# Optimization experiments

Hardware: AMD Instinct MI355X
Metric: run time of the kernel (lower is better)

Reference implementation:

```python
import jax, jax.numpy as jnp
import numpy as np

# Qwen3-MoE style config
B, S, D = 2, 2048, 2048        # batch, seqlen, hidden_size
E, I, TOPK = 64, 768, 8        # num_experts, moe_intermediate_size, num_experts_per_tok
M = B * S                      # tokens
CAP = 2 * (M * TOPK) // E


def setup_inputs() -> dict:
    key = jax.random.key(0)
    k0, k1, k2, k3, k4 = jax.random.split(key, 5)
    return {
        "x": jax.random.normal(k0, (B, S, D), jnp.float32),
        "router_weight": jax.random.normal(k1, (D, E), jnp.float32) * 0.02,
        "gate_proj": jax.random.normal(k2, (E, D, I), jnp.float32) * 0.02,
        "up_proj": jax.random.normal(k3, (E, D, I), jnp.float32) * 0.02,
        "down_proj": jax.random.normal(k4, (E, I, D), jnp.float32) * 0.02,
    }


def _moe(x, router_weight, gate_proj, up_proj, down_proj):
    b, s, d = x.shape
    xf = x.reshape(-1, d)                                  # [M, d]
    m = xf.shape[0]

    # ---- TokenChoiceTopKRouter: softmax scores, top-k, renormalize ----
    logits = xf @ router_weight                            # [M, E]
    probs = jax.nn.softmax(logits.astype(jnp.float32), axis=-1)
    topw, topi = jax.lax.top_k(probs, TOPK)                # [M, k]
    topw = topw / topw.sum(axis=-1, keepdims=True)         # norm_topk_prob

    flat_e = topi.reshape(-1)                              # [M*k] expert id per assignment
    flat_w = topw.reshape(-1).astype(x.dtype)              # [M*k] routing weight per assignment

    # ---- permute: sort assignments by expert (stable) ----
    order = jnp.argsort(flat_e)                            # [M*k]
    se = flat_e[order]                                     # sorted expert ids
    tok = order // TOPK                                    # source token per sorted assignment
    counts = jax.ops.segment_sum(jnp.ones_like(flat_e), flat_e, num_segments=E)
    starts = jnp.cumsum(counts) - counts                   # exclusive prefix sum
    pos = jnp.arange(m * TOPK) - starts[se]                # slot within expert's buffer
    valid = pos < CAP
    posc = jnp.minimum(pos, CAP - 1)

    # ---- dispatch to padded per-expert buffers [E, CAP, d] ----
    xe = jnp.zeros((E, CAP, d), x.dtype).at[se, pos].set(xf[tok], mode='drop')

    # ---- grouped SwiGLU experts (batched GEMMs) ----
    h = jax.nn.silu(jnp.einsum('ecd,edi->eci', xe, gate_proj)) \
        * jnp.einsum('ecd,edi->eci', xe, up_proj)          # [E, CAP, I]
    ye = jnp.einsum('eci,eid->ecd', h, down_proj)          # [E, CAP, d]

    # ---- unpermute + weighted combine ----
    contrib = jnp.where(valid[:, None], ye[se, posc], 0.0) * flat_w[order][:, None]
    out = jnp.zeros((m, d), x.dtype).at[tok].add(contrib)  # sum over topk per token
    return out.reshape(b, s, d)


def reference(x, router_weight, gate_proj, up_proj, down_proj):
    return _moe(x, router_weight, gate_proj, up_proj, down_proj)
```

## Files before the change

### kernel.cpp

```cpp
#include <hip/hip_runtime.h>
#include <hip/hip_bf16.h>

typedef __attribute__((ext_vector_type(4))) float f32x4;
typedef __attribute__((ext_vector_type(8))) short bf16x8;
typedef __attribute__((ext_vector_type(8))) unsigned short us8;
typedef unsigned int   u32;
typedef unsigned short u16;

#define D_DIM 2048
#define I_DIM 768
#define NE    64
#define CAP   1024
#define NTOK  4096

__device__ __forceinline__ u32 cvt2(float a, float b) {
  __hip_bfloat162 hh = __float22bfloat162_rn(float2{a, b});
  union { __hip_bfloat162 h; u32 u; } c; c.h = hh; return c.u;
}
__device__ __forceinline__ u16 f2b(float f) {
  __hip_bfloat16 b = __float2bfloat16(f);
  union { __hip_bfloat16 b; u16 u; } c; c.b = b; return c.u;
}
__device__ __forceinline__ float b2f(u16 v) {
  union { u32 u; float f; } c; c.u = (u32)v << 16; return c.f;
}
__device__ __forceinline__ void glp16(const void* g, void* l) {
  __builtin_amdgcn_global_load_lds(
      (const __attribute__((address_space(1))) u32*)g,
      (__attribute__((address_space(3))) u32*)l, 16, 0, 0);
}

#define VMW(n) asm volatile("s_waitcnt vmcnt(" #n ")" ::: "memory")
#define BARF   do { __builtin_amdgcn_s_barrier(); \
                    asm volatile("" ::: "memory"); } while (0)

__global__ __launch_bounds__(256) void k_cvt_x(const float* __restrict__ x,
                                               u16* __restrict__ xb) {
  const size_t i = ((size_t)blockIdx.x * 256 + threadIdx.x) * 8;
  float4 v0 = *(const float4*)(x + i);
  float4 v1 = *(const float4*)(x + i + 4);
  uint4 o;
  o.x = cvt2(v0.x, v0.y); o.y = cvt2(v0.z, v0.w);
  o.z = cvt2(v1.x, v1.y); o.w = cvt2(v1.z, v1.w);
  *(uint4*)(xb + i) = o;
}

__global__ __launch_bounds__(256) void k_router(
    const float* __restrict__ x, const float* __restrict__ rw,
    int* __restrict__ counts, int* __restrict__ slot_token,
    float* __restrict__ slot_w)
{
  const int lane = threadIdx.x & 63;
  const int tok  = blockIdx.x * 4 + (threadIdx.x >> 6);
  const float* xr = x + (size_t)tok * D_DIM;

  float acc = 0.f;
  for (int d0 = 0; d0 < D_DIM; d0 += 64) {
    float xv = xr[d0 + lane];
    #pragma unroll
    for (int j = 0; j < 64; ++j) {
      float xj = __shfl(xv, j, 64);
      acc = fmaf(xj, rw[(size_t)(d0 + j) * NE + lane], acc);
    }
  }

  float v = acc; int vi = lane;
  float wk[8]; int ei[8];
  float mx0 = 0.f, wsum = 0.f;
  #pragma unroll
  for (int k = 0; k < 8; ++k) {
    float mv = v; int mi = vi;
    #pragma unroll
    for (int off = 32; off >= 1; off >>= 1) {
      float ov = __shfl_xor(mv, off, 64);
      int   oi = __shfl_xor(mi, off, 64);
      if (ov > mv || (ov == mv && oi < mi)) { mv = ov; mi = oi; }
    }
    if (k == 0) mx0 = mv;
    float ew = __expf(mv - mx0);
    wk[k] = ew; ei[k] = mi; wsum += ew;
    if (lane == mi) v = -3.4e38f;
  }

  if (lane == 0) {
    float inv = 1.f / wsum;
    #pragma unroll
    for (int k = 0; k < 8; ++k) {
      int ee   = ei[k];
      int slot = atomicAdd(&counts[ee], 1);
      if (slot < CAP) {
        slot_token[ee * CAP + slot] = tok;
        slot_w[ee * CAP + slot]     = wk[k] * inv;
      }
    }
  }
}

__global__ __launch_bounds__(256) void k_inv(
    const int* __restrict__ counts, const int* __restrict__ slot_token,
    int* __restrict__ tok_cnt, int* __restrict__ tok_idx)
{
  const int e = blockIdx.x;
  int cnt = counts[e]; if (cnt > CAP) cnt = CAP;
  for (int s = threadIdx.x; s < cnt; s += 256) {
    const int tok = slot_token[e * CAP + s];
    const int pos = atomicAdd(&tok_cnt[tok], 1);
    if (pos < 8) tok_idx[tok * 8 + pos] = e * CAP + s;
  }
}

__global__ __launch_bounds__(256) void k_wpack(const float* __restrict__ in,
                                               u16* __restrict__ outp,
                                               int R, int C) {
  const int e  = blockIdx.z;
  const int c0 = blockIdx.x * 64;
  const int r0 = blockIdx.y * 64;
  const float* ip = in + (size_t)e * R * C;
  u16* op = outp + (size_t)e * (size_t)(C / 64) * (R / 8) * 512
                 + ((size_t)(c0 / 64) * (R / 8) + (r0 / 8)) * 512;

  __shared__ u16 T[64][76];
  const int t  = threadIdx.x;
  const int rr = t >> 4;
  const int cc = (t & 15) * 4;
  #pragma unroll
  for (int it = 0; it < 4; ++it) {
    const int r = rr + it * 16;
    float4 v = *(const float4*)(ip + (size_t)(r0 + r) * C + c0 + cc);
    T[cc + 0][r] = f2b(v.x);
    T[cc + 1][r] = f2b(v.y);
    T[cc + 2][r] = f2b(v.z);
    T[cc + 3][r] = f2b(v.w);
  }
  __syncthreads();
  const int n = t & 63;
  #pragma unroll
  for (int p = 0; p < 2; ++p) {
    const int c = (t >> 6) + p * 4;
    const u16* s = &T[n][c * 8];
    uint4 o;
    o.x = (u32)s[0] | ((u32)s[1] << 16);
    o.y = (u32)s[2] | ((u32)s[3] << 16);
    o.z = (u32)s[4] | ((u32)s[5] << 16);
    o.w = (u32)s[6] | ((u32)s[7] << 16);
    *(uint4*)(op + ((size_t)c * 64 + n) * 8) = o;
  }
}

__global__ __launch_bounds__(256) void k_xpack(
    const u16* __restrict__ xb, const int* __restrict__ counts,
    const int* __restrict__ slot_token, u16* __restrict__ xeT)
{
  const int e   = blockIdx.z;
  const int s0  = blockIdx.y * 64;
  const int kc0 = blockIdx.x * 32;
  int cnt = counts[e]; if (cnt > CAP) cnt = CAP;

  __shared__ u16 T[64][264];
  const int t = threadIdx.x;
  const int r = t >> 2;
  const int q = t & 3;
  const int  tok  = slot_token[e * CAP + s0 + r];
  const bool live = (s0 + r) < cnt;
  const u16* src = xb + (size_t)tok * D_DIM + kc0 * 8;

  #pragma unroll
  for (int it = 0; it < 8; ++it) {
    const int kl = it * 32 + q * 8;
    us8 v = {0, 0, 0, 0, 0, 0, 0, 0};
    if (live) v = *(const us8*)(src + kl);
    *(us8*)&T[r][kl] = v;
  }
  __syncthreads();

  u16* dst = xeT + (size_t)e * 2097152 + (size_t)kc0 * 8192 + (size_t)s0 * 8;
  const int sl = t & 63;
  #pragma unroll
  for (int p = 0; p < 8; ++p) {
    const int c = (t >> 6) + p * 4;
    const u16* s = &T[sl][c * 8];
    uint4 o = *(const uint4*)s;
    *(uint4*)(dst + (size_t)c * 8192 + sl * 8) = o;
  }
}


__device__ __forceinline__ void m1_issue(
    const u16* xeA, const u16* gb, const u16* ub, u16* st,
    int js, int wv, int lane, int m0)
{
  #pragma unroll
  for (int q = 0; q < 6; ++q) {
    const int id = wv * 6 + q;
    const int kc = (id >> 1) & 3;
    const int h  = id & 1;
    const size_t kcA = (size_t)(js * 4 + kc);
    if (id < 8) {
      glp16(xeA + kcA * 8192 + (size_t)(m0 + h * 64 + lane) * 8,
            st + kc * 1024 + h * 512);
    } else if (id < 16) {
      glp16(gb + (size_t)h * 131072 + kcA * 512 + lane * 8,
            st + 4096 + kc * 1024 + h * 512);
    } else {
      glp16(ub + (size_t)h * 131072 + kcA * 512 + lane * 8,
            st + 8192 + kc * 1024 + h * 512);
    }
  }
}

__device__ __forceinline__ void m1_step(
    const u16* st, int gq, int li, int mrow, int icol,
    f32x4 (&ag)[4][4], f32x4 (&au)[4][4])
{
  bf16x8 a[4], g[4], u[4];
  #pragma unroll
  for (int mf = 0; mf < 4; ++mf)
    a[mf] = *(const bf16x8*)&st[(gq * 128 + mrow + mf * 16 + li) * 8];
  #pragma unroll
  for (int nf = 0; nf < 4; ++nf) {
    g[nf] = *(const bf16x8*)&st[4096 + (gq * 128 + icol + nf * 16 + li) * 8];
    u[nf] = *(const bf16x8*)&st[8192 + (gq * 128 + icol + nf * 16 + li) * 8];
  }
  __builtin_amdgcn_s_setprio(1);
  #pragma unroll
  for (int mf = 0; mf < 4; ++mf)
    #pragma unroll
    for (int nf = 0; nf < 4; ++nf) {
      ag[mf][nf] = __builtin_amdgcn_mfma_f32_16x16x32_bf16(a[mf], g[nf], ag[mf][nf], 0, 0, 0);
      au[mf][nf] = __builtin_amdgcn_mfma_f32_16x16x32_bf16(a[mf], u[nf], au[mf][nf], 0, 0, 0);
    }
  __builtin_amdgcn_s_setprio(0);
}

__global__ __launch_bounds__(256, 2) void k_mlp1p(
    const u16* __restrict__ xeT, const u16* __restrict__ Gpk,
    const u16* __restrict__ Upk, const int* __restrict__ counts,
    u16* __restrict__ hP)
{
  extern __shared__ u16 sm[];
  const int i   = blockIdx.x;
  const int xcd = i & 7;
  const int p   = i >> 3;
  const int mt  = p & 7;
  const int pe  = p >> 3;
  const int val = pe * 8 + xcd;
  const int e   = val / 6;
  const int nt  = val % 6;

  int cnt = counts[e]; if (cnt > CAP) cnt = CAP;
  const int m0 = mt * 128;
  if (m0 >= cnt) return;

  const int t = threadIdx.x;
  const int lane = t & 63, wv = t >> 6;
  const int li = lane & 15, gq = lane >> 4;
  const int mrow = (wv >> 1) * 64, icol = (wv & 1) * 64;

  const u16* xeA = xeT + (size_t)e * 2097152;
  const u16* gb  = Gpk + (size_t)e * 1572864 + (size_t)(nt * 2) * 131072;
  const u16* ub  = Upk + (size_t)e * 1572864 + (size_t)(nt * 2) * 131072;
  u16* hPe = hP + (size_t)e * 786432;

  f32x4 ag[4][4], au[4][4];
  #pragma unroll
  for (int mf = 0; mf < 4; ++mf)
    #pragma unroll
    for (int nf = 0; nf < 4; ++nf) {
      f32x4 z = {0.f, 0.f, 0.f, 0.f};
      ag[mf][nf] = z; au[mf][nf] = z;
    }

  m1_issue(xeA, gb, ub, sm,         0, wv, lane, m0);
  m1_issue(xeA, gb, ub, sm + 12288, 1, wv, lane, m0);

  for (int j = 0; j < 62; ++j) {
    VMW(6); BARF;
    m1_issue(xeA, gb, ub, sm + ((j + 2) % 3) * 12288, j + 2, wv, lane, m0);
    m1_step(sm + (j % 3) * 12288, gq, li, mrow, icol, ag, au);
  }
  VMW(6); BARF; m1_step(sm + 2 * 12288, gq, li, mrow, icol, ag, au);
  VMW(0); BARF; m1_step(sm + 0 * 12288, gq, li, mrow, icol, ag, au);

  #pragma unroll
  for (int mf = 0; mf < 4; ++mf)
    #pragma unroll
    for (int jj = 0; jj < 4; ++jj) {
      const int slot = m0 + mrow + mf * 16 + gq * 4 + jj;
      #pragma unroll
      for (int nf = 0; nf < 4; ++nf) {
        const int ii = nt * 128 + icol + nf * 16 + li;
        float gg = ag[mf][nf][jj];
        float uu = au[mf][nf][jj];
        hPe[(size_t)(ii >> 3) * 8192 + slot * 8 + (ii & 7)] =
            f2b(gg * uu / (1.f + __expf(-gg)));
      }
    }
}

__device__ __forceinline__ void m2_issue(
    const u16* hPe, const u16* dp, u16* st,
    int js, int wv, int lane, int m0)
{
  #pragma unroll
  for (int q = 0; q < 6; ++q) {
    const int id = wv * 6 + q;
    const size_t kcA = (size_t)(js * 4 + ((id < 8) ? ((id >> 1) & 3) : ((id - 8) & 3)));
    if (id < 8) {
      const int kc = (id >> 1) & 3;
      const int h  = id & 1;
      glp16(hPe + kcA * 8192 + (size_t)(m0 + h * 64 + lane) * 8,
            st + kc * 1024 + h * 512);
    } else {
      const int r  = id - 8;
      const int kc = r & 3;
      const int ng = r >> 2;
      glp16(dp + (size_t)ng * 49152 + kcA * 512 + lane * 8,
            st + 4096 + kc * 2048 + ng * 512);
    }
  }
}

__device__ __forceinline__ void m2_step(
    const u16* st, int gq, int li, int mrow, int ncol,
    f32x4 (&acc)[4][8])
{
  bf16x8 a[4], b[8];
  #pragma unroll
  for (int mf = 0; mf < 4; ++mf)
    a[mf] = *(const bf16x8*)&st[(gq * 128 + mrow + mf * 16 + li) * 8];
  #pragma unroll
  for (int nf = 0; nf < 8; ++nf)
    b[nf] = *(const bf16x8*)&st[4096 + (gq * 256 + ncol + nf * 16 + li) * 8];
  __builtin_amdgcn_s_setprio(1);
  #pragma unroll
  for (int mf = 0; mf < 4; ++mf)
    #pragma unroll
    for (int nf = 0; nf < 8; ++nf)
      acc[mf][nf] = __builtin_amdgcn_mfma_f32_16x16x32_bf16(a[mf], b[nf], acc[mf][nf], 0, 0, 0);
  __builtin_amdgcn_s_setprio(0);
}

__global__ __launch_bounds__(256, 2) void k_mlp2p(
    const u16* __restrict__ hP, const u16* __restrict__ Dpk,
    const int* __restrict__ counts, const float* __restrict__ slot_w,
    u16* __restrict__ ye)
{
  extern __shared__ u16 sm[];
  const int i   = blockIdx.x;
  const int xcd = i & 7;
  const int p   = i >> 3;
  const int mt  = p & 7;
  const int pe  = p >> 3;
  const int val = pe * 8 + xcd;
  const int e   = val >> 3;
  const int nt  = val & 7;

  int cnt = counts[e]; if (cnt > CAP) cnt = CAP;
  const int m0 = mt * 128;
  if (m0 >= cnt) return;
  const int n0 = nt * 256;

  const int t = threadIdx.x;
  const int lane = t & 63, wv = t >> 6;
  const int li = lane & 15, gq = lane >> 4;
  const int mrow = (wv >> 1) * 64, ncol = (wv & 1) * 128;

  const u16* hPe = hP + (size_t)e * 786432;
  const u16* dp  = Dpk + (size_t)e * 1572864 + (size_t)(nt * 4) * 49152;
  const int eCAP = e * CAP;

  f32x4 acc[4][8];
  #pragma unroll
  for (int mf = 0; mf < 4; ++mf)
    #pragma unroll
    for (int nf = 0; nf < 8; ++nf) { f32x4 z = {0.f,0.f,0.f,0.f}; acc[mf][nf] = z; }

  m2_issue(hPe, dp, sm,         0, wv, lane, m0);
  m2_issue(hPe, dp, sm + 12288, 1, wv, lane, m0);

  for (int j = 0; j < 22; ++j) {
    VMW(6); BARF;
    m2_issue(hPe, dp, sm + ((j + 2) % 3) * 12288, j + 2, wv, lane, m0);
    m2_step(sm + (j % 3) * 12288, gq, li, mrow, ncol, acc);
  }
  VMW(6); BARF; m2_step(sm + (22 % 3) * 12288, gq, li, mrow, ncol, acc);
  VMW(0); BARF; m2_step(sm + (23 % 3) * 12288, gq, li, mrow, ncol, acc);

  #pragma unroll
  for (int mf = 0; mf < 4; ++mf)
    #pragma unroll
    for (int jj = 0; jj < 4; ++jj) {
      const int slot = m0 + mrow + mf * 16 + gq * 4 + jj;
      if (slot < cnt) {
        const float wgt = slot_w[eCAP + slot];
        u16* yr = ye + (size_t)(eCAP + slot) * D_DIM + n0 + ncol + li;
        #pragma unroll
        for (int nf = 0; nf < 8; ++nf)
          yr[nf * 16] = f2b(wgt * acc[mf][nf][jj]);
      }
    }
}

__global__ __launch_bounds__(256) void k_combine(
    const u16* __restrict__ ye, const int* __restrict__ tok_idx,
    const int* __restrict__ tok_cnt, float* __restrict__ out)
{
  const int tok = blockIdx.x;
  const int c0  = threadIdx.x * 8;
  int cnt8 = tok_cnt[tok]; if (cnt8 > 8) cnt8 = 8;

  float s[8] = {0.f, 0.f, 0.f, 0.f, 0.f, 0.f, 0.f, 0.f};
  #pragma unroll
  for (int k = 0; k < 8; ++k) {
    if (k < cnt8) {
      const int idx = tok_idx[tok * 8 + k];
      const us8 v = *(const us8*)(ye + (size_t)idx * D_DIM + c0);
      #pragma unroll
      for (int j = 0; j < 8; ++j) s[j] += b2f(v[j]);
    }
  }
  float4 o0 = {s[0], s[1], s[2], s[3]};
  float4 o1 = {s[4], s[5], s[6], s[7]};
  float* op = out + (size_t)tok * D_DIM + c0;
  *(float4*)op       = o0;
  *(float4*)(op + 4) = o1;
}

extern "C" void kernel_launch(void* const* d_in, const int* in_sizes, int n_in,
                              void* d_out, int out_size, void* d_ws, size_t ws_size,
                              hipStream_t stream) {
  const float* x    = (const float*)d_in[0];
  const float* rw   = (const float*)d_in[1];
  const float* gate = (const float*)d_in[2];
  const float* up   = (const float*)d_in[3];
  const float* down = (const float*)d_in[4];
  float* out = (float*)d_out;

  char* ws = (char*)d_ws;
  int*   counts     = (int*)ws;
  int*   slot_token = (int*)(ws + 1024);
  float* slot_w     = (float*)(ws + 263168);
  u16*   xb         = (u16*)(ws + 525312);
  u16*   hP         = (u16*)(ws + 17302528);
  u16*   Gpk        = (u16*)(ws + 117965824);
  u16*   Upk        = (u16*)(ws + 319292416);
  u16*   xeT        = (u16*)(ws + 520619008);
  u16*   Dpk        = xeT;
  u16*   ye         = Gpk;
  int*   tok_cnt    = (int*)(ws + 721945600);
  int*   tok_idx    = (int*)(ws + 721945600 + 16384);

  hipFuncSetAttribute((const void*)k_mlp1p,
                      hipFuncAttributeMaxDynamicSharedMemorySize, 73728);
  hipFuncSetAttribute((const void*)k_mlp2p,
                      hipFuncAttributeMaxDynamicSharedMemorySize, 73728);

  hipMemsetAsync(counts, 0, NE * sizeof(int), stream);
  hipMemsetAsync(slot_token, 0, (size_t)NE * CAP * sizeof(int), stream);

  k_cvt_x <<<dim3((NTOK * D_DIM) / (256 * 8)), 256, 0, stream>>>(x, xb);
  k_router<<<dim3(NTOK / 4),                   256, 0, stream>>>(x, rw, counts, slot_token, slot_w);

  k_wpack<<<dim3(12, 32, NE), 256, 0, stream>>>(gate, Gpk, D_DIM, I_DIM);
  k_wpack<<<dim3(12, 32, NE), 256, 0, stream>>>(up,   Upk, D_DIM, I_DIM);
  k_xpack<<<dim3(8, 16, NE),  256, 0, stream>>>(xb, counts, slot_token, xeT);
  k_mlp1p<<<dim3(3072), 256, 73728, stream>>>(xeT, Gpk, Upk, counts, hP);

  hipMemsetAsync(tok_cnt, 0, NTOK * sizeof(int), stream);
  k_inv  <<<dim3(NE), 256, 0, stream>>>(counts, slot_token, tok_cnt, tok_idx);
  k_wpack<<<dim3(32, 12, NE), 256, 0, stream>>>(down, Dpk, I_DIM, D_DIM);

  k_mlp2p  <<<dim3(4096), 256, 73728, stream>>>(hP, Dpk, counts, slot_w, ye);
  k_combine<<<dim3(NTOK), 256, 0, stream>>>(ye, tok_idx, tok_cnt, out);
}
```

Baseline: 1.191 ms.

## Software-pipeline LDS fragment loads with MFMA via double-buffered registers in expert GEMMs

Splits each GEMM step into an LDS-to-register load and an MFMA phase, then double-buffers register fragments so the LDS reads for the next k-step are issued while MFMAs run on the previous step's fragments. Both the gate/up GEMM and the down GEMM get this restructured, manually unrolled schedule with an explicit lgkmcnt wait before each barrier. The aim is to hide LDS read latency behind matrix-core work. The cost is a second set of fragment registers, which adds pressure under launch bounds of 2 blocks per CU and could cause spills or lower occupancy.

```diff
diff --git a/kernel.cpp b/kernel.cpp
--- a/kernel.cpp
+++ b/kernel.cpp
@@ -31,6 +31,7 @@
 }
 
 #define VMW(n) asm volatile("s_waitcnt vmcnt(" #n ")" ::: "memory")
+#define LGK    asm volatile("s_waitcnt lgkmcnt(0)" ::: "memory")
 #define BARF   do { __builtin_amdgcn_s_barrier(); \
                     asm volatile("" ::: "memory"); } while (0)
 
@@ -184,6 +185,8 @@
   }
 }
 
+
+struct M1R { bf16x8 a[4]; bf16x8 g[4]; bf16x8 u[4]; };
 
 __device__ __forceinline__ void m1_issue(
     const u16* xeA, const u16* gb, const u16* ub, u16* st,
@@ -208,26 +211,29 @@
   }
 }
 
-__device__ __forceinline__ void m1_step(
-    const u16* st, int gq, int li, int mrow, int icol,
-    f32x4 (&ag)[4][4], f32x4 (&au)[4][4])
-{
-  bf16x8 a[4], g[4], u[4];
-  #pragma unroll
-  for (int mf = 0; mf < 4; ++mf)
-    a[mf] = *(const bf16x8*)&st[(gq * 128 + mrow + mf * 16 + li) * 8];
+__device__ __forceinline__ void m1_load(
+    M1R& r, const u16* st, int gq, int li, int mrow, int icol)
+{
+  #pragma unroll
+  for (int mf = 0; mf < 4; ++mf)
+    r.a[mf] = *(const bf16x8*)&st[(gq * 128 + mrow + mf * 16 + li) * 8];
   #pragma unroll
   for (int nf = 0; nf < 4; ++nf) {
-    g[nf] = *(const bf16x8*)&st[4096 + (gq * 128 + icol + nf * 16 + li) * 8];
-    u[nf] = *(const bf16x8*)&st[8192 + (gq * 128 + icol + nf * 16 + li) * 8];
-  }
+    r.g[nf] = *(const bf16x8*)&st[4096 + (gq * 128 + icol + nf * 16 + li) * 8];
+    r.u[nf] = *(const bf16x8*)&st[8192 + (gq * 128 + icol + nf * 16 + li) * 8];
+  }
+}
+
+__device__ __forceinline__ void m1_mma(
+    const M1R& r, f32x4 (&ag)[4][4], f32x4 (&au)[4][4])
+{
   __builtin_amdgcn_s_setprio(1);
   #pragma unroll
   for (int mf = 0; mf < 4; ++mf)
     #pragma unroll
     for (int nf = 0; nf < 4; ++nf) {
-      ag[mf][nf] = __builtin_amdgcn_mfma_f32_16x16x32_bf16(a[mf], g[nf], ag[mf][nf], 0, 0, 0);
-      au[mf][nf] = __builtin_amdgcn_mfma_f32_16x16x32_bf16(a[mf], u[nf], au[mf][nf], 0, 0, 0);
+      ag[mf][nf] = __builtin_amdgcn_mfma_f32_16x16x32_bf16(r.a[mf], r.g[nf], ag[mf][nf], 0, 0, 0);
+      au[mf][nf] = __builtin_amdgcn_mfma_f32_16x16x32_bf16(r.a[mf], r.u[nf], au[mf][nf], 0, 0, 0);
     }
   __builtin_amdgcn_s_setprio(0);
 }
@@ -270,16 +276,35 @@
       ag[mf][nf] = z; au[mf][nf] = z;
     }
 
+  M1R R0, R1;
+  int js = 0;
+
+#define M1PH(WAITN, DO_ISS, ISSBUF, LDBUF, RLD, RMM)                      \
+  do {                                                                    \
+    LGK; VMW(WAITN); BARF;                                                \
+    if (DO_ISS) { m1_issue(xeA, gb, ub, sm + (ISSBUF) * 12288, js, wv, lane, m0); ++js; } \
+    m1_load(RLD, sm + (LDBUF) * 12288, gq, li, mrow, icol);               \
+    if (RMM) m1_mma(*(RMM), ag, au);                                      \
+  } while (0)
+
   m1_issue(xeA, gb, ub, sm,         0, wv, lane, m0);
   m1_issue(xeA, gb, ub, sm + 12288, 1, wv, lane, m0);
-
-  for (int j = 0; j < 62; ++j) {
-    VMW(6); BARF;
-    m1_issue(xeA, gb, ub, sm + ((j + 2) % 3) * 12288, j + 2, wv, lane, m0);
-    m1_step(sm + (j % 3) * 12288, gq, li, mrow, icol, ag, au);
-  }
-  VMW(6); BARF; m1_step(sm + 2 * 12288, gq, li, mrow, icol, ag, au);
-  VMW(0); BARF; m1_step(sm + 0 * 12288, gq, li, mrow, icol, ag, au);
+  js = 2;
+
+  M1PH(6, true, 2, 0, R0, (M1R*)0);
+  for (int jt = 0; jt < 10; ++jt) {
+    M1PH(6, true, 0, 1, R1, &R0);
+    M1PH(6, true, 1, 2, R0, &R1);
+    M1PH(6, true, 2, 0, R1, &R0);
+    M1PH(6, true, 0, 1, R0, &R1);
+    M1PH(6, true, 1, 2, R1, &R0);
+    M1PH(6, true, 2, 0, R0, &R1);
+  }
+  M1PH(6, true, 0, 1, R1, &R0);
+  M1PH(6, false, 0, 2, R0, &R1);
+  M1PH(0, false, 0, 0, R1, &R0);
+  m1_mma(R1, ag, au);
+#undef M1PH
 
   #pragma unroll
   for (int mf = 0; mf < 4; ++mf)
@@ -296,6 +321,8 @@
       }
     }
 }
+
+struct M2R { bf16x8 a[4]; bf16x8 b[8]; };
 
 __device__ __forceinline__ void m2_issue(
     const u16* hPe, const u16* dp, u16* st,
@@ -320,23 +347,25 @@
   }
 }
 
-__device__ __forceinline__ void m2_step(
-    const u16* st, int gq, int li, int mrow, int ncol,
-    f32x4 (&acc)[4][8])
-{
-  bf16x8 a[4], b[8];
-  #pragma unroll
-  for (int mf = 0; mf < 4; ++mf)
-    a[mf] = *(const bf16x8*)&st[(gq * 128 + mrow + mf * 16 + li) * 8];
+__device__ __forceinline__ void m2_load(
+    M2R& r, const u16* st, int gq, int li, int mrow, int ncol)
+{
+  #pragma unroll
+  for (int mf = 0; mf < 4; ++mf)
+    r.a[mf] = *(const bf16x8*)&st[(gq * 128 + mrow + mf * 16 + li) * 8];
   #pragma unroll
   for (int nf = 0; nf < 8; ++nf)
-    b[nf] = *(const bf16x8*)&st[4096 + (gq * 256 + ncol + nf * 16 + li) * 8];
+    r.b[nf] = *(const bf16x8*)&st[4096 + (gq * 256 + ncol + nf * 16 + li) * 8];
+}
+
+__device__ __forceinline__ void m2_mma(const M2R& r, f32x4 (&acc)[4][8])
+{
   __builtin_amdgcn_s_setprio(1);
   #pragma unroll
   for (int mf = 0; mf < 4; ++mf)
     #pragma unroll
     for (int nf = 0; nf < 8; ++nf)
-      acc[mf][nf] = __builtin_amdgcn_mfma_f32_16x16x32_bf16(a[mf], b[nf], acc[mf][nf], 0, 0, 0);
+      acc[mf][nf] = __builtin_amdgcn_mfma_f32_16x16x32_bf16(r.a[mf], r.b[nf], acc[mf][nf], 0, 0, 0);
   __builtin_amdgcn_s_setprio(0);
 }
 
@@ -375,16 +404,37 @@
     #pragma unroll
     for (int nf = 0; nf < 8; ++nf) { f32x4 z = {0.f,0.f,0.f,0.f}; acc[mf][nf] = z; }
 
+  M2R R0, R1;
+  int js = 0;
+
+#define M2PH(WAITN, DO_ISS, ISSBUF, LDBUF, RLD, RMM)                      \
+  do {                                                                    \
+    LGK; VMW(WAITN); BARF;                                                \
+    if (DO_ISS) { m2_issue(hPe, dp, sm + (ISSBUF) * 12288, js, wv, lane, m0); ++js; } \
+    m2_load(RLD, sm + (LDBUF) * 12288, gq, li, mrow, ncol);               \
+    if (RMM) m2_mma(*(RMM), acc);                                         \
+  } while (0)
+
   m2_issue(hPe, dp, sm,         0, wv, lane, m0);
   m2_issue(hPe, dp, sm + 12288, 1, wv, lane, m0);
-
-  for (int j = 0; j < 22; ++j) {
-    VMW(6); BARF;
-    m2_issue(hPe, dp, sm + ((j + 2) % 3) * 12288, j + 2, wv, lane, m0);
-    m2_step(sm + (j % 3) * 12288, gq, li, mrow, ncol, acc);
-  }
-  VMW(6); BARF; m2_step(sm + (22 % 3) * 12288, gq, li, mrow, ncol, acc);
-  VMW(0); BARF; m2_step(sm + (23 % 3) * 12288, gq, li, mrow, ncol, acc);
+  js = 2;
+
+  M2PH(6, true, 2, 0, R0, (M2R*)0);
+  for (int jt = 0; jt < 3; ++jt) {
+    M2PH(6, true, 0, 1, R1, &R0);
+    M2PH(6, true, 1, 2, R0, &R1);
+    M2PH(6, true, 2, 0, R1, &R0);
+    M2PH(6, true, 0, 1, R0, &R1);
+    M2PH(6, true, 1, 2, R1, &R0);
+    M2PH(6, true, 2, 0, R0, &R1);
+  }
+  M2PH(6, true, 0, 1, R1, &R0);
+  M2PH(6, true, 1, 2, R0, &R1);
+  M2PH(6, true, 2, 0, R1, &R0);
+  M2PH(6, false, 0, 1, R0, &R1);
+  M2PH(0, false, 0, 2, R1, &R0);
+  m2_mma(R1, acc);
+#undef M2PH
 
   #pragma unroll
   for (int mf = 0; mf < 4; ++mf)
```

New measurement: 2.988 ms. 151% more time.
